# Kernel optimization log

Measured on AMD Instinct MI355X. Metric: run time of the kernel, lower is better.

The kernel has to match this reference:

```python
import jax, jax.numpy as jnp
import numpy as np
from jax import lax

BN_EPS = 1e-5


def _zpool(x, axis):
    # stack (mean, max) over `axis` as 2 channels -> [N, 2, A, B]
    return jnp.stack([jnp.mean(x, axis=axis), jnp.max(x, axis=axis)], axis=1)


def _gate(p2, conv_w, conv_b, bn_w, bn_b, bn_rm, bn_rv, i):
    # p2: [N, 2, A, B]; 7x7 conv (2->1, pad 3) + scalar BN + relu + sigmoid
    y = lax.conv_general_dilated(
        p2, conv_w, window_strides=(1, 1), padding=[(3, 3), (3, 3)],
        dimension_numbers=("NCHW", "OIHW", "NCHW"))[:, 0] + conv_b[0]  # [N, A, B]
    y = (y - bn_rm[i]) * lax.rsqrt(bn_rv[i] + BN_EPS) * bn_w[i] + bn_b[i]
    return jax.nn.sigmoid(jnp.maximum(y, 0.0))


def setup_inputs() -> dict:
    key = jax.random.key(0)
    ks = jax.random.split(key, 7)
    N, C, H, W = 256, 2048, 7, 7
    return {
        "x": jax.random.normal(ks[0], (N, C, H, W), dtype=jnp.float32),
        "conv_w": jax.random.normal(ks[1], (1, 2, 7, 7), dtype=jnp.float32) * 0.1,
        "conv_b": jax.random.normal(ks[2], (1,), dtype=jnp.float32) * 0.1,
        "bn_w": jax.random.normal(ks[3], (3,), dtype=jnp.float32),
        "bn_b": jax.random.normal(ks[4], (3,), dtype=jnp.float32),
        "bn_rm": jax.random.normal(ks[5], (3,), dtype=jnp.float32) * 0.1,
        "bn_rv": jax.random.uniform(ks[6], (3,), dtype=jnp.float32),
    }


def reference(x, conv_w, conv_b, bn_w, bn_b, bn_rm, bn_rv):
    # x: [N, C, 7, 7]
    g_hw = _gate(_zpool(x, 1), conv_w, conv_b, bn_w, bn_b, bn_rm, bn_rv, 0)  # [N, 7, 7]
    g_ch = _gate(_zpool(x, 3), conv_w, conv_b, bn_w, bn_b, bn_rm, bn_rv, 1)  # [N, C, 7] indexed by h
    g_cw = _gate(_zpool(x, 2), conv_w, conv_b, bn_w, bn_b, bn_rm, bn_rv, 2)  # [N, C, 7] indexed by w
    gate = (g_hw[:, None, :, :] + g_ch[:, :, :, None] + g_cw[:, :, None, :]) * (1.0 / 3.0)
    return x * gate
```

## Files before the change

kernel.cpp:

```cpp
#include <hip/hip_runtime.h>

#define N_ 256
#define C_ 2048
#define HW_ 49
#define CPB 64
#define NCHUNK 8

#define CHB(lc) ((lc) * HW_ + ((lc) >= 3 ? 1 : 0))

__global__ __launch_bounds__(256) void k_poolc(const float* __restrict__ x,
                                               float* __restrict__ psum,
                                               float* __restrict__ pmax) {
  const int bc = blockIdx.x, n = blockIdx.y;
  const int t = threadIdx.x;
  __shared__ __align__(16) float sx[CPB * HW_];
  __shared__ float part_s[HW_][5];
  __shared__ float part_m[HW_][5];

  float sm = 0.f, mx = -3.4e38f;
  const int hw = t / 5, s = t % 5;

  const float4* xv = (const float4*)(x + ((size_t)n * C_ + (size_t)bc * 256) * HW_);
  #pragma unroll
  for (int pass = 0; pass < 4; ++pass) {
    float4* sv = (float4*)sx;
    for (int v = t; v < 784; v += 256) sv[v] = xv[pass * 784 + v];
    __syncthreads();
    if (t < 245) {
      #pragma unroll
      for (int j = 0; j < 13; ++j) {
        int c = s * 13 + j;
        if (c < CPB) { float a = sx[c * HW_ + hw]; sm += a; mx = fmaxf(mx, a); }
      }
    }
    __syncthreads();
  }
  if (t < 245) { part_s[hw][s] = sm; part_m[hw][s] = mx; }
  __syncthreads();
  if (t < HW_) {
    float s2 = 0.f, m2 = -3.4e38f;
    #pragma unroll
    for (int k = 0; k < 5; ++k) { s2 += part_s[t][k]; m2 = fmaxf(m2, part_m[t][k]); }
    size_t o = ((size_t)n * NCHUNK + bc) * HW_ + t;
    psum[o] = s2; pmax[o] = m2;
  }
}

__global__ __launch_bounds__(64) void k_ghw(const float* __restrict__ psum,
                                            const float* __restrict__ pmax,
                                            const float* __restrict__ cw,
                                            const float* __restrict__ cb,
                                            const float* __restrict__ bnw,
                                            const float* __restrict__ bnb,
                                            const float* __restrict__ bnrm,
                                            const float* __restrict__ bnrv,
                                            float* __restrict__ ghw) {
  const int n = blockIdx.x;
  const int t = threadIdx.x;
  __shared__ float p2c[2][13][13];
  __shared__ float s_cw[98];

  for (int i = t; i < 2 * 13 * 13; i += 64) ((float*)p2c)[i] = 0.f;
  for (int i = t; i < 98; i += 64) s_cw[i] = cw[i];
  __syncthreads();

  if (t < HW_) {
    float sm = 0.f, mx = -3.4e38f;
    const float* ps = psum + (size_t)n * NCHUNK * HW_ + t;
    const float* pm = pmax + (size_t)n * NCHUNK * HW_ + t;
    #pragma unroll
    for (int cc = 0; cc < NCHUNK; ++cc) {
      sm += ps[cc * HW_];
      mx = fmaxf(mx, pm[cc * HW_]);
    }
    p2c[0][t / 7 + 3][t % 7 + 3] = sm * (1.f / C_);
    p2c[1][t / 7 + 3][t % 7 + 3] = mx;
  }
  __syncthreads();

  if (t < HW_) {
    int a = t / 7, b = t % 7;
    float y = cb[0];
    #pragma unroll
    for (int i2 = 0; i2 < 2; ++i2)
      #pragma unroll
      for (int p = 0; p < 7; ++p)
        #pragma unroll
        for (int q = 0; q < 7; ++q)
          y += p2c[i2][a + p][b + q] * s_cw[i2 * 49 + p * 7 + q];
    float sc = bnw[0] * rsqrtf(bnrv[0] + 1e-5f);
    y = (y - bnrm[0]) * sc + bnb[0];
    y = fmaxf(y, 0.f);
    ghw[n * HW_ + t] = 1.f / (1.f + __expf(-y));
  }
}

__global__ __launch_bounds__(256, 4) void k_main_p(const float* __restrict__ x,
    const float* __restrict__ ghw,
    const float* __restrict__ cw, const float* __restrict__ cb,
    const float* __restrict__ bnw, const float* __restrict__ bnb,
    const float* __restrict__ bnrm, const float* __restrict__ bnrv,
    float* __restrict__ out) {
  const int bx = blockIdx.x;
  const int n  = (N_ - 1) - blockIdx.y;
  const int t  = threadIdx.x;

  __shared__ __align__(16) float sx[2][3432];
  __shared__ __align__(16) float pool_lo[1120];
  __shared__ __align__(16) float pool_hi[1120];
  __shared__ float gch[448];
  __shared__ float gcw[448];
  __shared__ __align__(16) float s_w[112];
  __shared__ float s_ghw[49];

  const int conv = t & 1, i2 = (t >> 1) & 1, cl = t >> 2;
  const int bi = 1 + conv;
  const float cb0 = cb[0];
  const float sc_bn = bnw[bi] * rsqrtf(bnrv[bi] + 1e-5f);
  const float rm_bn = bnrm[bi];
  const float sh_bn = bnb[bi];

  if (t < 112) {
    int i2w = t / 56, rem = t % 56, p = rem / 8, q = rem % 8;
    s_w[t] = (q < 7) ? cw[i2w * 49 + p * 7 + q] : 0.f;
  }
  if (t < HW_) s_ghw[t] = ghw[n * HW_ + t];
  {
    const int c0 = (bx * 4) * CPB;
    for (int i = t; i < 294; i += 256) {
      int side = i / 147, off = i % 147;
      int lc = side ? (67 + off / HW_) : (off / HW_);
      int c = c0 - 3 + lc;
      float vv = 0.f;
      if (c >= 0 && c < C_) vv = x[((size_t)n * C_ + c) * HW_ + off % HW_];
      sx[0][CHB(lc) + off % HW_] = vv;
    }
    const float4* xv = (const float4*)(x + ((size_t)n * C_ + c0) * HW_);
    float4* sxv = (float4*)(&sx[0][148]);
    for (int v = t; v < 784; v += 256) sxv[v] = xv[v];
  }
  __syncthreads();

  #pragma unroll
  for (int j = 0; j < 4; ++j) {
    const int cur = j & 1, nxt = cur ^ 1;
    const int cc = bx * 4 + j;
    const int c0 = cc * CPB;
    float* sxc = sx[cur];

    float4 q0, q1, q2, q3;
    float h0, h1;
    if (j < 3) {
      const int c0n = (cc + 1) * CPB;
      const float4* xvn = (const float4*)(x + ((size_t)n * C_ + c0n) * HW_);
      if (t < 196) { q0 = xvn[t]; q1 = xvn[t + 196]; q2 = xvn[t + 392]; q3 = xvn[t + 588]; }
      if (t < 147) {
        int lcl = t / 49, off = t % 49;
        int cl_ = c0n - 3 + lcl;
        int ch_ = c0n + CPB + lcl;
        h0 = (cl_ >= 0 && cl_ < C_) ? x[((size_t)n * C_ + cl_) * HW_ + off] : 0.f;
        h1 = (ch_ < C_) ? x[((size_t)n * C_ + ch_) * HW_ + off] : 0.f;
      }
    }

    for (int i = t; i < 70 * 7; i += 256) {
      int lc = i / 7, k = i % 7;
      int base = CHB(lc);
      float s1 = 0.f, m1 = -3.4e38f, s2 = 0.f, m2 = -3.4e38f;
      #pragma unroll
      for (int jj = 0; jj < 7; ++jj) {
        float a = sxc[base + k * 7 + jj]; s1 += a; m1 = fmaxf(m1, a);
        float b = sxc[base + jj * 7 + k]; s2 += b; m2 = fmaxf(m2, b);
      }
      float* pb = (k < 4) ? pool_lo : pool_hi;
      int kk = k & 3;
      pb[(0 * 70 + lc) * 4 + kk] = s1 * (1.f / 7.f);
      pb[(1 * 70 + lc) * 4 + kk] = m1;
      pb[(2 * 70 + lc) * 4 + kk] = s2 * (1.f / 7.f);
      pb[(3 * 70 + lc) * 4 + kk] = m2;
    }
    __syncthreads();

    {
      const int f = conv * 2 + i2;
      const float* Wb = s_w + i2 * 56;
      float acc[7] = {0.f, 0.f, 0.f, 0.f, 0.f, 0.f, 0.f};
      #pragma unroll
      for (int p = 0; p < 7; ++p) {
        int ri = (f * 70 + cl + p) * 4;
        float4 r0 = *(const float4*)(pool_lo + ri);
        float4 r1 = *(const float4*)(pool_hi + ri);
        float row[7] = {r0.x, r0.y, r0.z, r0.w, r1.x, r1.y, r1.z};
        float4 w0 = *(const float4*)(Wb + p * 8);
        float4 w1 = *(const float4*)(Wb + p * 8 + 4);
        float wr[7] = {w0.x, w0.y, w0.z, w0.w, w1.x, w1.y, w1.z};
        #pragma unroll
        for (int q = 0; q < 7; ++q)
          #pragma unroll
          for (int k = 0; k < 7; ++k) {
            int c = k + q - 3;
            if (c >= 0 && c < 7) acc[k] += row[c] * wr[q];
          }
      }
      float fsum[7];
      #pragma unroll
      for (int k = 0; k < 7; ++k) fsum[k] = acc[k] + __shfl_xor(acc[k], 2, 64);
      if (i2 == 0) {
        float* gp = (conv ? gcw : gch) + cl * 7;
        #pragma unroll
        for (int k = 0; k < 7; ++k) {
          float y = (fsum[k] + cb0 - rm_bn) * sc_bn + sh_bn;
          y = fmaxf(y, 0.f);
          gp[k] = 1.f / (1.f + __expf(-y));
        }
      }
    }

    if (j < 3) {
      float* sxn = sx[nxt];
      float4* sxnv = (float4*)(sxn + 148);
      if (t < 196) { sxnv[t] = q0; sxnv[t + 196] = q1; sxnv[t + 392] = q2; sxnv[t + 588] = q3; }
      if (t < 147) {
        int lcl = t / 49, off = t % 49;
        sxn[CHB(lcl) + off] = h0;
        sxn[CHB(67 + lcl) + off] = h1;
      }
    }
    __syncthreads();

    {
      const float4* sxv = (const float4*)(sxc + 148);
      float4* outv = (float4*)(out + ((size_t)n * C_ + c0) * HW_);
      for (int v = t; v < 784; v += 256) {
        float4 q = sxv[v];
        int e0 = v * 4;
        int cj = e0 / 49;
        int hw0 = e0 - cj * 49;
        float r[4] = {q.x, q.y, q.z, q.w};
        #pragma unroll
        for (int jj = 0; jj < 4; ++jj) {
          int hw = hw0 + jj;
          int cjj = cj + (hw >= 49);
          hw -= (hw >= 49) ? 49 : 0;
          int h = (hw * 37) >> 8, w2 = hw - h * 7;
          r[jj] *= (s_ghw[hw] + gch[cjj * 7 + h] + gcw[cjj * 7 + w2]) * (1.f / 3.f);
        }
        outv[v] = make_float4(r[0], r[1], r[2], r[3]);
      }
    }
  }
}

extern "C" void kernel_launch(void* const* d_in, const int* in_sizes, int n_in,
                              void* d_out, int out_size, void* d_ws, size_t ws_size,
                              hipStream_t stream) {
  const float* x    = (const float*)d_in[0];
  const float* cw   = (const float*)d_in[1];
  const float* cb   = (const float*)d_in[2];
  const float* bnw  = (const float*)d_in[3];
  const float* bnb  = (const float*)d_in[4];
  const float* bnrm = (const float*)d_in[5];
  const float* bnrv = (const float*)d_in[6];
  float* out = (float*)d_out;

  float* psum = (float*)d_ws;
  float* pmax = psum + (size_t)N_ * NCHUNK * HW_;
  float* ghw  = pmax + (size_t)N_ * NCHUNK * HW_;

  k_poolc<<<dim3(NCHUNK, N_), 256, 0, stream>>>(x, psum, pmax);
  k_ghw<<<dim3(N_), 64, 0, stream>>>(psum, pmax, cw, cb, bnw, bnb, bnrm, bnrv, ghw);
  k_main_p<<<dim3(NCHUNK, N_), 256, 0, stream>>>(x, ghw, cw, cb, bnw, bnb, bnrm,
                                                 bnrv, out);
}
```

Before: 76.96 us.

## Replace pipelined 256-thread main kernel with single-wave 16-channel blocks

The main gating kernel is rewritten so each 64-thread block handles 16 channels for one sample, giving 128x256 blocks instead of 8x256 large double-buffered blocks. Halo channels for the channel-axis convolution are pooled directly from global memory instead of being staged in shared memory. The output pass re-reads x from global (likely L2) rather than shared memory. This trades the explicit load/compute pipelining for much higher block-level parallelism and less shared memory per block, at the cost of redundant halo loads and reading x twice.

```diff
diff --git a/kernel.cpp b/kernel.cpp
--- a/kernel.cpp
+++ b/kernel.cpp
@@ -3,17 +3,17 @@
 #define N_ 256
 #define C_ 2048
 #define HW_ 49
-#define CPB 64
 #define NCHUNK 8
-
-#define CHB(lc) ((lc) * HW_ + ((lc) >= 3 ? 1 : 0))
+#define CPT 16
+#define NCT (C_/CPT)
+#define PSTRIDE 184
 
 __global__ __launch_bounds__(256) void k_poolc(const float* __restrict__ x,
                                                float* __restrict__ psum,
                                                float* __restrict__ pmax) {
   const int bc = blockIdx.x, n = blockIdx.y;
   const int t = threadIdx.x;
-  __shared__ __align__(16) float sx[CPB * HW_];
+  __shared__ __align__(16) float sx[64 * HW_];
   __shared__ float part_s[HW_][5];
   __shared__ float part_m[HW_][5];
 
@@ -30,7 +30,7 @@
       #pragma unroll
       for (int j = 0; j < 13; ++j) {
         int c = s * 13 + j;
-        if (c < CPB) { float a = sx[c * HW_ + hw]; sm += a; mx = fmaxf(mx, a); }
+        if (c < 64) { float a = sx[c * HW_ + hw]; sm += a; mx = fmaxf(mx, a); }
       }
     }
     __syncthreads();
@@ -95,158 +95,143 @@
   }
 }
 
-__global__ __launch_bounds__(256, 4) void k_main_p(const float* __restrict__ x,
+__global__ __launch_bounds__(64) void k_w64(const float* __restrict__ x,
     const float* __restrict__ ghw,
     const float* __restrict__ cw, const float* __restrict__ cb,
     const float* __restrict__ bnw, const float* __restrict__ bnb,
     const float* __restrict__ bnrm, const float* __restrict__ bnrv,
     float* __restrict__ out) {
-  const int bx = blockIdx.x;
+  const int bc = blockIdx.x;
   const int n  = (N_ - 1) - blockIdx.y;
-  const int t  = threadIdx.x;
-
-  __shared__ __align__(16) float sx[2][3432];
-  __shared__ __align__(16) float pool_lo[1120];
-  __shared__ __align__(16) float pool_hi[1120];
-  __shared__ float gch[448];
-  __shared__ float gcw[448];
+  const int c0 = bc * CPT;
+  const int lane = threadIdx.x;
+
+  __shared__ __align__(16) float sx[CPT * 52];
+  __shared__ __align__(16) float pools[4 * PSTRIDE];
   __shared__ __align__(16) float s_w[112];
+  __shared__ float gch[112];
+  __shared__ float gcw[112];
   __shared__ float s_ghw[49];
 
-  const int conv = t & 1, i2 = (t >> 1) & 1, cl = t >> 2;
-  const int bi = 1 + conv;
-  const float cb0 = cb[0];
-  const float sc_bn = bnw[bi] * rsqrtf(bnrv[bi] + 1e-5f);
-  const float rm_bn = bnrm[bi];
-  const float sh_bn = bnb[bi];
-
-  if (t < 112) {
-    int i2w = t / 56, rem = t % 56, p = rem / 8, q = rem % 8;
-    s_w[t] = (q < 7) ? cw[i2w * 49 + p * 7 + q] : 0.f;
-  }
-  if (t < HW_) s_ghw[t] = ghw[n * HW_ + t];
+  for (int i = lane; i < 112; i += 64) {
+    int i2w = i / 56, rem = i % 56, p = rem / 8, q = rem % 8;
+    s_w[i] = (q < 7) ? cw[i2w * 49 + p * 7 + q] : 0.f;
+  }
+  if (lane < HW_) s_ghw[lane] = ghw[n * HW_ + lane];
+  const float4* xv = (const float4*)(x + ((size_t)n * C_ + c0) * HW_);
+  #pragma unroll
+  for (int m = 0; m < 4; ++m) {
+    int v = lane + m * 64;
+    if (v < 196) {
+      float4 q = xv[v];
+      int e = v * 4, ch = e / 49, pos = e - ch * 49;
+      int base = ch * 52 + pos;
+      sx[base] = q.x;
+      sx[base + 1 + ((pos >= 48) ? 3 : 0)] = q.y;
+      sx[base + 2 + ((pos >= 47) ? 3 : 0)] = q.z;
+      sx[base + 3 + ((pos >= 46) ? 3 : 0)] = q.w;
+    }
+  }
+  __syncthreads();
+
+  #pragma unroll
+  for (int it = 0; it < 3; ++it) {
+    int i = lane + it * 64;
+    if (i < 154) {
+      int ch = i / 7, k = i % 7;
+      float s1 = 0.f, m1, s2 = 0.f, m2;
+      if (ch >= 3 && ch < 19) {
+        int base = (ch - 3) * 52;
+        m1 = -3.4e38f; m2 = -3.4e38f;
+        #pragma unroll
+        for (int j = 0; j < 7; ++j) {
+          float a = sx[base + k * 7 + j]; s1 += a; m1 = fmaxf(m1, a);
+          float b = sx[base + j * 7 + k]; s2 += b; m2 = fmaxf(m2, b);
+        }
+        s1 *= (1.f / 7.f); s2 *= (1.f / 7.f);
+      } else {
+        int c = c0 - 3 + ch;
+        bool ok = (c >= 0 && c < C_);
+        m1 = ok ? -3.4e38f : 0.f; m2 = m1;
+        if (ok) {
+          const float* xp = x + ((size_t)n * C_ + c) * HW_;
+          #pragma unroll
+          for (int j = 0; j < 7; ++j) {
+            float a = xp[k * 7 + j]; s1 += a; m1 = fmaxf(m1, a);
+            float b = xp[j * 7 + k]; s2 += b; m2 = fmaxf(m2, b);
+          }
+          s1 *= (1.f / 7.f); s2 *= (1.f / 7.f);
+        }
+      }
+      pools[0 * PSTRIDE + ch * 8 + k] = s1;
+      pools[1 * PSTRIDE + ch * 8 + k] = m1;
+      pools[2 * PSTRIDE + ch * 8 + k] = s2;
+      pools[3 * PSTRIDE + ch * 8 + k] = m2;
+    }
+  }
+  __syncthreads();
+
   {
-    const int c0 = (bx * 4) * CPB;
-    for (int i = t; i < 294; i += 256) {
-      int side = i / 147, off = i % 147;
-      int lc = side ? (67 + off / HW_) : (off / HW_);
-      int c = c0 - 3 + lc;
-      float vv = 0.f;
-      if (c >= 0 && c < C_) vv = x[((size_t)n * C_ + c) * HW_ + off % HW_];
-      sx[0][CHB(lc) + off % HW_] = vv;
-    }
-    const float4* xv = (const float4*)(x + ((size_t)n * C_ + c0) * HW_);
-    float4* sxv = (float4*)(&sx[0][148]);
-    for (int v = t; v < 784; v += 256) sxv[v] = xv[v];
-  }
-  __syncthreads();
-
-  #pragma unroll
-  for (int j = 0; j < 4; ++j) {
-    const int cur = j & 1, nxt = cur ^ 1;
-    const int cc = bx * 4 + j;
-    const int c0 = cc * CPB;
-    float* sxc = sx[cur];
-
-    float4 q0, q1, q2, q3;
-    float h0, h1;
-    if (j < 3) {
-      const int c0n = (cc + 1) * CPB;
-      const float4* xvn = (const float4*)(x + ((size_t)n * C_ + c0n) * HW_);
-      if (t < 196) { q0 = xvn[t]; q1 = xvn[t + 196]; q2 = xvn[t + 392]; q3 = xvn[t + 588]; }
-      if (t < 147) {
-        int lcl = t / 49, off = t % 49;
-        int cl_ = c0n - 3 + lcl;
-        int ch_ = c0n + CPB + lcl;
-        h0 = (cl_ >= 0 && cl_ < C_) ? x[((size_t)n * C_ + cl_) * HW_ + off] : 0.f;
-        h1 = (ch_ < C_) ? x[((size_t)n * C_ + ch_) * HW_ + off] : 0.f;
-      }
-    }
-
-    for (int i = t; i < 70 * 7; i += 256) {
-      int lc = i / 7, k = i % 7;
-      int base = CHB(lc);
-      float s1 = 0.f, m1 = -3.4e38f, s2 = 0.f, m2 = -3.4e38f;
-      #pragma unroll
-      for (int jj = 0; jj < 7; ++jj) {
-        float a = sxc[base + k * 7 + jj]; s1 += a; m1 = fmaxf(m1, a);
-        float b = sxc[base + jj * 7 + k]; s2 += b; m2 = fmaxf(m2, b);
-      }
-      float* pb = (k < 4) ? pool_lo : pool_hi;
-      int kk = k & 3;
-      pb[(0 * 70 + lc) * 4 + kk] = s1 * (1.f / 7.f);
-      pb[(1 * 70 + lc) * 4 + kk] = m1;
-      pb[(2 * 70 + lc) * 4 + kk] = s2 * (1.f / 7.f);
-      pb[(3 * 70 + lc) * 4 + kk] = m2;
-    }
-    __syncthreads();
-
-    {
-      const int f = conv * 2 + i2;
-      const float* Wb = s_w + i2 * 56;
-      float acc[7] = {0.f, 0.f, 0.f, 0.f, 0.f, 0.f, 0.f};
-      #pragma unroll
-      for (int p = 0; p < 7; ++p) {
-        int ri = (f * 70 + cl + p) * 4;
-        float4 r0 = *(const float4*)(pool_lo + ri);
-        float4 r1 = *(const float4*)(pool_hi + ri);
-        float row[7] = {r0.x, r0.y, r0.z, r0.w, r1.x, r1.y, r1.z};
-        float4 w0 = *(const float4*)(Wb + p * 8);
-        float4 w1 = *(const float4*)(Wb + p * 8 + 4);
-        float wr[7] = {w0.x, w0.y, w0.z, w0.w, w1.x, w1.y, w1.z};
-        #pragma unroll
-        for (int q = 0; q < 7; ++q)
-          #pragma unroll
-          for (int k = 0; k < 7; ++k) {
-            int c = k + q - 3;
-            if (c >= 0 && c < 7) acc[k] += row[c] * wr[q];
-          }
-      }
-      float fsum[7];
-      #pragma unroll
-      for (int k = 0; k < 7; ++k) fsum[k] = acc[k] + __shfl_xor(acc[k], 2, 64);
-      if (i2 == 0) {
-        float* gp = (conv ? gcw : gch) + cl * 7;
+    const int cl = lane >> 2, conv = (lane >> 1) & 1, i2 = lane & 1;
+    const int f = conv * 2 + i2;
+    const float* Wb = s_w + i2 * 56;
+    float acc[7] = {0.f, 0.f, 0.f, 0.f, 0.f, 0.f, 0.f};
+    #pragma unroll
+    for (int p = 0; p < 7; ++p) {
+      int ri = f * PSTRIDE + (cl + p) * 8;
+      float4 r0 = *(const float4*)(pools + ri);
+      float4 r1 = *(const float4*)(pools + ri + 4);
+      float row[7] = {r0.x, r0.y, r0.z, r0.w, r1.x, r1.y, r1.z};
+      float4 w0 = *(const float4*)(Wb + p * 8);
+      float4 w1 = *(const float4*)(Wb + p * 8 + 4);
+      float wr[7] = {w0.x, w0.y, w0.z, w0.w, w1.x, w1.y, w1.z};
+      #pragma unroll
+      for (int q = 0; q < 7; ++q)
         #pragma unroll
         for (int k = 0; k < 7; ++k) {
-          float y = (fsum[k] + cb0 - rm_bn) * sc_bn + sh_bn;
-          y = fmaxf(y, 0.f);
-          gp[k] = 1.f / (1.f + __expf(-y));
+          int c = k + q - 3;
+          if (c >= 0 && c < 7) acc[k] += row[c] * wr[q];
         }
-      }
-    }
-
-    if (j < 3) {
-      float* sxn = sx[nxt];
-      float4* sxnv = (float4*)(sxn + 148);
-      if (t < 196) { sxnv[t] = q0; sxnv[t + 196] = q1; sxnv[t + 392] = q2; sxnv[t + 588] = q3; }
-      if (t < 147) {
-        int lcl = t / 49, off = t % 49;
-        sxn[CHB(lcl) + off] = h0;
-        sxn[CHB(67 + lcl) + off] = h1;
-      }
-    }
-    __syncthreads();
-
-    {
-      const float4* sxv = (const float4*)(sxc + 148);
-      float4* outv = (float4*)(out + ((size_t)n * C_ + c0) * HW_);
-      for (int v = t; v < 784; v += 256) {
-        float4 q = sxv[v];
-        int e0 = v * 4;
-        int cj = e0 / 49;
-        int hw0 = e0 - cj * 49;
-        float r[4] = {q.x, q.y, q.z, q.w};
-        #pragma unroll
-        for (int jj = 0; jj < 4; ++jj) {
-          int hw = hw0 + jj;
-          int cjj = cj + (hw >= 49);
-          hw -= (hw >= 49) ? 49 : 0;
-          int h = (hw * 37) >> 8, w2 = hw - h * 7;
-          r[jj] *= (s_ghw[hw] + gch[cjj * 7 + h] + gcw[cjj * 7 + w2]) * (1.f / 3.f);
-        }
-        outv[v] = make_float4(r[0], r[1], r[2], r[3]);
-      }
+    }
+    float fsum[7];
+    #pragma unroll
+    for (int k = 0; k < 7; ++k) fsum[k] = acc[k] + __shfl_xor(acc[k], 1, 64);
+    const int bi = 1 + conv;
+    const float cb0 = cb[0];
+    const float sc_bn = bnw[bi] * rsqrtf(bnrv[bi] + 1e-5f);
+    const float rm_bn = bnrm[bi];
+    const float sh_bn = bnb[bi];
+    if (i2 == 0) {
+      float* gp = (conv ? gcw : gch) + cl * 7;
+      #pragma unroll
+      for (int k = 0; k < 7; ++k) {
+        float y = (fsum[k] + cb0 - rm_bn) * sc_bn + sh_bn;
+        y = fmaxf(y, 0.f);
+        gp[k] = 1.f / (1.f + __expf(-y));
+      }
+    }
+  }
+  __syncthreads();
+
+  float4* outv = (float4*)(out + ((size_t)n * C_ + c0) * HW_);
+  #pragma unroll
+  for (int m = 0; m < 4; ++m) {
+    int v = lane + m * 64;
+    if (v < 196) {
+      float4 q = xv[v];
+      int e0 = v * 4;
+      int cj = e0 / 49;
+      int hw0 = e0 - cj * 49;
+      float r[4] = {q.x, q.y, q.z, q.w};
+      #pragma unroll
+      for (int j = 0; j < 4; ++j) {
+        int hw = hw0 + j;
+        int cjj = cj + (hw >= 49);
+        hw -= (hw >= 49) ? 49 : 0;
+        int h = (hw * 37) >> 8, w2 = hw - h * 7;
+        r[j] *= (s_ghw[hw] + gch[cjj * 7 + h] + gcw[cjj * 7 + w2]) * (1.f / 3.f);
+      }
+      outv[v] = make_float4(r[0], r[1], r[2], r[3]);
     }
   }
 }
@@ -269,6 +254,5 @@
 
   k_poolc<<<dim3(NCHUNK, N_), 256, 0, stream>>>(x, psum, pmax);
   k_ghw<<<dim3(N_), 64, 0, stream>>>(psum, pmax, cw, cb, bnw, bnb, bnrm, bnrv, ghw);
-  k_main_p<<<dim3(NCHUNK, N_), 256, 0, stream>>>(x, ghw, cw, cb, bnw, bnb, bnrm,
-                                                 bnrv, out);
-}
+  k_w64<<<dim3(NCT, N_), 64, 0, stream>>>(x, ghw, cw, cb, bnw, bnb, bnrm, bnrv, out);
+}
```

Result: slower. 86.76 us (+12.7%).
